# Kernel optimization log

Measured on AMD Instinct MI355X. Metric: run time of the kernel, lower is better.

## Reference

```python
import jax, jax.numpy as jnp
import numpy as np
from jax import lax

N, D_IN, D_H, D_A, N_CLS, K = 50000, 1024, 512, 256, 2, 8


def setup_inputs() -> dict:
    key = jax.random.key(0)
    ks = jax.random.split(key, 13)
    s = 0.02
    return {
        "h": jax.random.normal(ks[0], (1, N, D_IN), dtype=jnp.float32),
        "fc_W": jax.random.normal(ks[1], (D_H, D_IN), dtype=jnp.float32) * s,
        "fc_b": jnp.zeros((D_H,), jnp.float32),
        "att_a_W": jax.random.normal(ks[2], (D_A, D_H), dtype=jnp.float32) * s,
        "att_a_b": jnp.zeros((D_A,), jnp.float32),
        "att_b_W": jax.random.normal(ks[3], (D_A, D_H), dtype=jnp.float32) * s,
        "att_b_b": jnp.zeros((D_A,), jnp.float32),
        "att_c_W": jax.random.normal(ks[4], (1, D_A), dtype=jnp.float32) * s,
        "att_c_b": jnp.zeros((1,), jnp.float32),
        "cls_W": jax.random.normal(ks[5], (N_CLS, D_H), dtype=jnp.float32) * s,
        "cls_b": jnp.zeros((N_CLS,), jnp.float32),
        "inst_W": jax.random.normal(ks[6], (2, D_H), dtype=jnp.float32) * s,
        "inst_b": jnp.zeros((2,), jnp.float32),
        "label": 1,  # one_hot -> [0,1]: inst_eval runs only for classifier index 1
    }


def reference(h, fc_W, fc_b, att_a_W, att_a_b, att_b_W, att_b_b,
              att_c_W, att_c_b, cls_W, cls_b, inst_W, inst_b, label):
    x = jnp.squeeze(h, 0)                               # [N, 1024]
    hh = jax.nn.relu(x @ fc_W.T + fc_b)                 # [N, 512]
    # gated attention: tanh gate * sigmoid gate -> scalar score per instance
    a = jnp.tanh(hh @ att_a_W.T + att_a_b)              # [N, 256]
    b = jax.nn.sigmoid(hh @ att_b_W.T + att_b_b)        # [N, 256]
    A_raw = (a * b) @ att_c_W.T + att_c_b               # [N, 1]
    A = jax.nn.softmax(A_raw, axis=0)                   # softmax over instances

    # instance eval (label==1, subtyping=False -> only classifier index 1)
    scores = A_raw[:, 0]                                # [N]
    _, top_p_ids = lax.top_k(scores, K)
    _, top_n_ids = lax.top_k(-scores, K)
    ids = jnp.concatenate([top_p_ids, top_n_ids])       # [2K]
    inst = hh[ids]                                      # gather [2K, 512]
    logits = inst @ inst_W.T + inst_b                   # [2K, 2]
    targets = jnp.concatenate([jnp.ones((K,), jnp.int32),
                               jnp.zeros((K,), jnp.int32)])
    logp = jax.nn.log_softmax(logits, axis=-1)
    instance_loss = -jnp.mean(jnp.take_along_axis(logp, targets[:, None], axis=1))

    instance_scores = hh @ cls_W.T + cls_b              # [N, 2]
    preds = (instance_scores * A).sum(axis=0) / A.sum(axis=0)  # [2]
    preds = preds[None, :]                              # [1, 2]
    return preds, instance_scores, A_raw, instance_loss
```

## Files before the change

### kernel.cpp

```cpp
#include <hip/hip_runtime.h>
#include <hip/hip_bf16.h>
#include <math.h>

typedef __bf16 bf16_t;
typedef __bf16 bf16x4 __attribute__((ext_vector_type(4)));
typedef __bf16 bf16x8 __attribute__((ext_vector_type(8)));
typedef float  f32x4  __attribute__((ext_vector_type(4)));

#define NROWS 50000

typedef const __attribute__((address_space(1))) unsigned int* gp_t;
typedef __attribute__((address_space(3))) unsigned int* lp_t;
__device__ __forceinline__ void cp16(void* l, const void* g) {
    __builtin_amdgcn_global_load_lds((gp_t)g, (lp_t)l, 16, 0, 0);
}

__global__ void k_convert(const float* __restrict__ fcW,
                          const float* __restrict__ aW,
                          const float* __restrict__ bW,
                          bf16_t* __restrict__ permW1, bf16_t* __restrict__ permB2) {
    int t = blockIdx.x * 256 + threadIdx.x;
    if (t < 131072) {
        float4 v = *(const float4*)(fcW + (long)t * 4);
        int row = t >> 8;
        int k0 = (t & 255) * 4;
        int kt = k0 >> 5, q = (k0 >> 3) & 3, j = k0 & 7;
        bf16_t o[4] = {(bf16_t)v.x, (bf16_t)v.y, (bf16_t)v.z, (bf16_t)v.w};
        *(bf16x4*)(permW1 + kt * 16384 + q * 4096 + row * 8 + j) = *(bf16x4*)o;
    } else {
        int t2 = t - 131072;
        int isB = t2 >> 15;
        int f = t2 & 32767;
        float4 v = *(const float4*)(((isB ? bW : aW)) + (long)f * 4);
        int srow = f >> 7;
        int k0 = (f & 127) * 4;
        int kt = k0 >> 5, q = (k0 >> 3) & 3, j = k0 & 7;
        int r = ((srow >> 4) * 2 + isB) * 16 + (srow & 15);
        bf16_t o[4] = {(bf16_t)v.x, (bf16_t)v.y, (bf16_t)v.z, (bf16_t)v.w};
        *(bf16x4*)(permB2 + kt * 16384 + q * 4096 + r * 8 + j) = *(bf16x4*)o;
    }
}

__global__ __launch_bounds__(256, 4) void k_gemm1(
        const float* __restrict__ x, const bf16_t* __restrict__ permW1,
        const float* __restrict__ fcb, bf16_t* __restrict__ hh) {
    __shared__ __align__(16) char smem[32768];
    const int tid = threadIdx.x;
    const int w = tid >> 6, l = tid & 63, q = l >> 4, li = l & 15;
    const int wr = w >> 1, wc = w & 1;
    const int b = blockIdx.x;
    const int rtile = (b & 7) | ((b >> 5) << 3);
    const int ctile = (b >> 3) & 3;
    const long row0 = (long)rtile * 128;
    const int col0 = ctile * 128;

    f32x4 acc[4][4];
    #pragma unroll
    for (int a = 0; a < 4; a++)
        #pragma unroll
        for (int c = 0; c < 4; c++) acc[a][c] = (f32x4)0.0f;

    int arow[4], akx[4]; bool avalid[4];
    #pragma unroll
    for (int j = 0; j < 4; j++) {
        int s = j * 256 + tid;
        arow[j] = s >> 3; akx[j] = s & 7;
        avalid[j] = (row0 + arow[j]) < NROWS;
    }
    const float* xbase = x + row0 * 1024;

    float4 xv[4];
    #pragma unroll
    for (int j = 0; j < 4; j++)
        xv[j] = avalid[j] ? *(const float4*)(xbase + arow[j] * 1024 + akx[j] * 4)
                          : make_float4(0.f, 0.f, 0.f, 0.f);
    #pragma unroll
    for (int j = 0; j < 4; j++) {
        bf16_t o[4] = {(bf16_t)xv[j].x, (bf16_t)xv[j].y, (bf16_t)xv[j].z, (bf16_t)xv[j].w};
        *(bf16x4*)(smem + (akx[j] >> 1) * 2048 + arow[j] * 16 + (akx[j] & 1) * 8) = *(bf16x4*)o;
    }
    #pragma unroll
    for (int s2 = 0; s2 < 2; s2++) {
        int s = tid + s2 * 256;
        cp16(smem + 16384 + s * 16, permW1 + (s >> 7) * 4096 + (col0 + (s & 127)) * 8);
    }
    #pragma unroll
    for (int j = 0; j < 4; j++)
        xv[j] = avalid[j] ? *(const float4*)(xbase + arow[j] * 1024 + 32 + akx[j] * 4)
                          : make_float4(0.f, 0.f, 0.f, 0.f);
    __syncthreads();

    for (int kt = 0; kt < 32; kt++) {
        const int cur = kt & 1, nxt = cur ^ 1;
        if (kt < 31) {
            const bf16_t* gsrc = permW1 + (long)(kt + 1) * 16384;
            #pragma unroll
            for (int s2 = 0; s2 < 2; s2++) {
                int s = tid + s2 * 256;
                cp16(smem + 16384 + nxt * 8192 + s * 16, gsrc + (s >> 7) * 4096 + (col0 + (s & 127)) * 8);
            }
            #pragma unroll
            for (int j = 0; j < 4; j++) {
                bf16_t o[4] = {(bf16_t)xv[j].x, (bf16_t)xv[j].y, (bf16_t)xv[j].z, (bf16_t)xv[j].w};
                *(bf16x4*)(smem + nxt * 8192 + (akx[j] >> 1) * 2048 + arow[j] * 16 + (akx[j] & 1) * 8) = *(bf16x4*)o;
            }
            int kn = (kt < 30 ? kt + 2 : 31) * 32;
            #pragma unroll
            for (int j = 0; j < 4; j++)
                xv[j] = avalid[j] ? *(const float4*)(xbase + arow[j] * 1024 + kn + akx[j] * 4)
                                  : make_float4(0.f, 0.f, 0.f, 0.f);
        }
        const bf16_t* Ab = (const bf16_t*)(smem + cur * 8192);
        const bf16_t* Bb = (const bf16_t*)(smem + 16384 + cur * 8192);
        bf16x8 afr[4], bfr[4];
        #pragma unroll
        for (int tn = 0; tn < 4; tn++)
            bfr[tn] = *(const bf16x8*)(Bb + q * 1024 + (wc * 64 + tn * 16 + li) * 8);
        #pragma unroll
        for (int tm = 0; tm < 4; tm++)
            afr[tm] = *(const bf16x8*)(Ab + q * 1024 + (wr * 64 + tm * 16 + li) * 8);
        #pragma unroll
        for (int tm = 0; tm < 4; tm++)
            #pragma unroll
            for (int tn = 0; tn < 4; tn++)
                acc[tm][tn] = __builtin_amdgcn_mfma_f32_16x16x32_bf16(afr[tm], bfr[tn], acc[tm][tn], 0, 0, 0);
        __syncthreads();
    }

    bf16_t* t16 = (bf16_t*)smem;
    float bias[4];
    #pragma unroll
    for (int tn = 0; tn < 4; tn++) bias[tn] = fcb[col0 + wc * 64 + tn * 16 + li];
    const int rr = tid >> 3, cc = tid & 7;
    #pragma unroll
    for (int tm = 0; tm < 4; tm++) {
        #pragma unroll
        for (int tn = 0; tn < 4; tn++)
            #pragma unroll
            for (int r = 0; r < 4; r++) {
                float v = acc[tm][tn][r] + bias[tn];
                v = v > 0.f ? v : 0.f;
                t16[(wr * 16 + q * 4 + r) * 136 + wc * 64 + tn * 16 + li] = (bf16_t)v;
            }
        __syncthreads();
        long grow = row0 + ((rr >> 4) * 64) + tm * 16 + (rr & 15);
        if (grow < NROWS) {
            bf16x8 v0 = *(const bf16x8*)&t16[rr * 136 + cc * 16];
            bf16x8 v1 = *(const bf16x8*)&t16[rr * 136 + cc * 16 + 8];
            *(bf16x8*)&hh[grow * 512 + col0 + cc * 16] = v0;
            *(bf16x8*)&hh[grow * 512 + col0 + cc * 16 + 8] = v1;
        }
        __syncthreads();
    }
}

__global__ __launch_bounds__(512, 4) void k_gemm2(
        const bf16_t* __restrict__ hh, const bf16_t* __restrict__ permB2,
        const float* __restrict__ aab, const float* __restrict__ abb,
        const float* __restrict__ acW, const float* __restrict__ acb,
        const float* __restrict__ clsW, const float* __restrict__ clsb,
        float* __restrict__ Araw, float* __restrict__ inst) {
    __shared__ __align__(16) char smem[75776];
    bf16_t* cls_lds = (bf16_t*)(smem + 73728);

    const int tid = threadIdx.x;
    const int w = tid >> 6, l = tid & 63, q = l >> 4, li = l & 15;
    const long row0 = (long)blockIdx.x * 64;

    if (tid < 128) {
        int c = tid >> 6, k8 = (tid & 63) * 8;
        #pragma unroll
        for (int i = 0; i < 8; i++)
            cls_lds[c * 512 + k8 + i] = (bf16_t)clsW[c * 512 + k8 + i];
    }

    f32x4 acc[4][4];
    #pragma unroll
    for (int a = 0; a < 4; a++)
        #pragma unroll
        for (int c = 0; c < 4; c++) acc[a][c] = (f32x4)0.0f;
    float cls0[4] = {0.f,0.f,0.f,0.f}, cls1[4] = {0.f,0.f,0.f,0.f};

    {
        const bf16_t* gb = permB2 + (long)tid * 8;
        char* dst = smem + 8192 + tid * 16;
        #pragma unroll
        for (int j = 0; j < 4; j++) cp16(dst + j * 8192, gb + j * 4096);
        if (tid < 256) {
            const bf16_t* ga = hh + (row0 + (tid >> 2)) * 512 + (tid & 3) * 8;
            cp16(smem + tid * 16, ga);
        }
    }
    __syncthreads();

    for (int kt = 0; kt < 16; kt++) {
        const int cur = kt & 1, nxt = cur ^ 1;
        if (kt < 15) {
            const bf16_t* gb = permB2 + ((long)(kt + 1) * 2048 + tid) * 8;
            char* dst = smem + 8192 + nxt * 32768 + tid * 16;
            #pragma unroll
            for (int j = 0; j < 4; j++) cp16(dst + j * 8192, gb + j * 4096);
            if (tid < 256) {
                const bf16_t* ga = hh + (row0 + (tid >> 2)) * 512 + (kt + 1) * 32 + (tid & 3) * 8;
                cp16(smem + nxt * 4096 + tid * 16, ga);
            }
        }
        const bf16_t* asb = (const bf16_t*)(smem + cur * 4096);
        const bf16_t* bsb = (const bf16_t*)(smem + 8192 + cur * 32768);
        bf16x8 bfr[4];
        #pragma unroll
        for (int tn = 0; tn < 4; tn++)
            bfr[tn] = *(const bf16x8*)(bsb + q * 4096 + (w * 64 + tn * 16 + li) * 8);
        const bool mycls = ((kt >> 1) == w);
        bf16x8 w0, w1;
        if (mycls) {
            w0 = *(const bf16x8*)&cls_lds[kt * 32 + q * 8];
            w1 = *(const bf16x8*)&cls_lds[512 + kt * 32 + q * 8];
        }
        #pragma unroll
        for (int tm = 0; tm < 4; tm++) {
            bf16x8 af = *(const bf16x8*)(asb + (tm * 16 + li) * 32 + q * 8);
            #pragma unroll
            for (int tn = 0; tn < 4; tn++)
                acc[tm][tn] = __builtin_amdgcn_mfma_f32_16x16x32_bf16(af, bfr[tn], acc[tm][tn], 0, 0, 0);
            if (mycls) {
                float s0 = 0.f, s1 = 0.f;
                #pragma unroll
                for (int jj = 0; jj < 8; jj++) {
                    float a = (float)af[jj];
                    s0 += a * (float)w0[jj];
                    s1 += a * (float)w1[jj];
                }
                cls0[tm] += s0; cls1[tm] += s1;
            }
        }
        __syncthreads();
    }

    float (*apart)[9] = (float (*)[9])smem;
    float (*cls_part)[64][2] = (float (*)[64][2])(smem + 4096);

    float sum_mr[4][4];
    #pragma unroll
    for (int a = 0; a < 4; a++)
        #pragma unroll
        for (int c = 0; c < 4; c++) sum_mr[a][c] = 0.f;
    #pragma unroll
    for (int p = 0; p < 2; p++) {
        int j = (w * 2 + p) * 16 + li;
        float ab_ = aab[j], bb_ = abb[j], cw = acW[j];
        int tn_a = p * 2, tn_b = p * 2 + 1;
        #pragma unroll
        for (int tm = 0; tm < 4; tm++)
            #pragma unroll
            for (int r = 0; r < 4; r++) {
                float av = tanhf(acc[tm][tn_a][r] + ab_);
                float bv = acc[tm][tn_b][r] + bb_;
                bv = 1.f / (1.f + expf(-bv));
                sum_mr[tm][r] += av * bv * cw;
            }
    }
    #pragma unroll
    for (int tm = 0; tm < 4; tm++)
        #pragma unroll
        for (int r = 0; r < 4; r++) {
            float v = sum_mr[tm][r];
            v += __shfl_xor(v, 1); v += __shfl_xor(v, 2);
            v += __shfl_xor(v, 4); v += __shfl_xor(v, 8);
            if (li == 0) apart[tm * 16 + q * 4 + r][w] = v;
        }
    #pragma unroll
    for (int tm = 0; tm < 4; tm++) {
        cls0[tm] += __shfl_xor(cls0[tm], 16); cls0[tm] += __shfl_xor(cls0[tm], 32);
        cls1[tm] += __shfl_xor(cls1[tm], 16); cls1[tm] += __shfl_xor(cls1[tm], 32);
        if (q == 0) {
            cls_part[w][tm * 16 + li][0] = cls0[tm];
            cls_part[w][tm * 16 + li][1] = cls1[tm];
        }
    }
    __syncthreads();
    if (tid < 64) {
        float s = acb[0];
        #pragma unroll
        for (int ww = 0; ww < 8; ww++) s += apart[tid][ww];
        long row = row0 + tid;
        if (row < NROWS) Araw[row] = s;
    }
    if (tid < 128) {
        int rr = tid >> 1, c = tid & 1;
        float s = clsb[c];
        #pragma unroll
        for (int ww = 0; ww < 8; ww++) s += cls_part[ww][rr][c];
        long row = row0 + rr;
        if (row < NROWS) inst[row * 2 + c] = s;
    }
}

__global__ void k_topk_part(const float* __restrict__ scores,
                            float* __restrict__ candV, int* __restrict__ candI,
                            float* __restrict__ sums) {
    __shared__ float cv[4096];
    __shared__ int   ci[4096];
    __shared__ float bwv[8]; __shared__ int bwi[8]; __shared__ int bws[8];
    int tid = threadIdx.x;
    int p = blockIdx.x;
    if (p == 0 && tid == 0) { sums[0] = 0.f; sums[1] = 0.f; sums[2] = 0.f; }
    int lo = p * 6250, hi = lo + 6250;
    for (int pass = 0; pass < 2; pass++) {
        float sign = (pass == 0) ? 1.f : -1.f;
        float tv[8]; int ti[8];
        #pragma unroll
        for (int k = 0; k < 8; k++) { tv[k] = -1e30f; ti[k] = 0x7fffffff; }
        for (int i = lo + tid; i < hi; i += 512) {
            float v = sign * scores[i];
            if (v > tv[7] || (v == tv[7] && i < ti[7])) {
                int k = 7;
                while (k > 0 && (v > tv[k-1] || (v == tv[k-1] && i < ti[k-1]))) {
                    tv[k] = tv[k-1]; ti[k] = ti[k-1]; k--;
                }
                tv[k] = v; ti[k] = i;
            }
        }
        for (int k = 0; k < 8; k++) { cv[tid * 8 + k] = tv[k]; ci[tid * 8 + k] = ti[k]; }
        __syncthreads();
        for (int r = 0; r < 8; r++) {
            float bv = -1e30f; int bi = 0x7fffffff, bslot = 0;
            for (int j = 0; j < 8; j++) {
                int s = tid + 512 * j;
                float v = cv[s]; int idx = ci[s];
                if (v > bv || (v == bv && idx < bi)) { bv = v; bi = idx; bslot = s; }
            }
            for (int m = 1; m < 64; m <<= 1) {
                float ov = __shfl_xor(bv, m); int oi = __shfl_xor(bi, m); int os = __shfl_xor(bslot, m);
                if (ov > bv || (ov == bv && oi < bi)) { bv = ov; bi = oi; bslot = os; }
            }
            if ((tid & 63) == 0) { bwv[tid >> 6] = bv; bwi[tid >> 6] = bi; bws[tid >> 6] = bslot; }
            __syncthreads();
            if (tid == 0) {
                float BV = -1e30f; int BI = 0x7fffffff, BS = 0;
                for (int wv = 0; wv < 8; wv++) {
                    if (bwv[wv] > BV || (bwv[wv] == BV && bwi[wv] < BI)) { BV = bwv[wv]; BI = bwi[wv]; BS = bws[wv]; }
                }
                candV[pass * 64 + p * 8 + r] = BV;
                candI[pass * 64 + p * 8 + r] = BI;
                cv[BS] = -1e30f; ci[BS] = 0x7fffffff;
            }
            __syncthreads();
        }
        __syncthreads();
    }
}

__global__ void k_sum(const float* __restrict__ Araw, const float* __restrict__ inst,
                      const float* __restrict__ candV, float* sums) {
    __shared__ float r0[4], r1[4], r2[4];
    int tid = threadIdx.x;
    float mx = -1e30f;
    #pragma unroll
    for (int p = 0; p < 8; p++) mx = fmaxf(mx, candV[p * 8]);
    float se = 0.f, s0 = 0.f, s1 = 0.f;
    for (int i = blockIdx.x * 256 + tid; i < NROWS; i += 32768) {
        float e = expf(Araw[i] - mx);
        se += e; s0 += inst[2 * i] * e; s1 += inst[2 * i + 1] * e;
    }
    for (int s = 1; s < 64; s <<= 1) {
        se += __shfl_xor(se, s); s0 += __shfl_xor(s0, s); s1 += __shfl_xor(s1, s);
    }
    if ((tid & 63) == 0) { r0[tid >> 6] = se; r1[tid >> 6] = s0; r2[tid >> 6] = s1; }
    __syncthreads();
    if (tid == 0) {
        atomicAdd(&sums[0], r0[0] + r0[1] + r0[2] + r0[3]);
        atomicAdd(&sums[1], r1[0] + r1[1] + r1[2] + r1[3]);
        atomicAdd(&sums[2], r2[0] + r2[1] + r2[2] + r2[3]);
    }
}

__global__ void k_fin(const bf16_t* __restrict__ hh,
                      const float* __restrict__ candV, const int* __restrict__ candI,
                      const float* __restrict__ sums, const float* __restrict__ instW,
                      const float* __restrict__ instb, float* __restrict__ dout) {
    __shared__ int mid[16];
    __shared__ float lg[16][2];
    int tid = threadIdx.x;
    int wv = tid >> 6, l = tid & 63;
    if (wv < 2) {
        float v = candV[wv * 64 + l];
        int idx = candI[wv * 64 + l];
        for (int r = 0; r < 8; r++) {
            float bv = v; int bi = idx; int bs = l;
            for (int m = 1; m < 64; m <<= 1) {
                float ov = __shfl_xor(bv, m); int oi = __shfl_xor(bi, m); int os = __shfl_xor(bs, m);
                if (ov > bv || (ov == bv && oi < bi)) { bv = ov; bi = oi; bs = os; }
            }
            if (l == 0) mid[wv * 8 + r] = bi;
            if (l == bs) v = -1e30f;
        }
    }
    __syncthreads();
    int r = tid >> 4, li = tid & 15;
    int id = mid[r];
    const bf16_t* hp = hh + (long)id * 512;
    float p0 = 0.f, p1 = 0.f;
    for (int k = li * 32; k < li * 32 + 32; k++) {
        float h = (float)hp[k];
        p0 += h * instW[k]; p1 += h * instW[512 + k];
    }
    for (int m = 1; m < 16; m <<= 1) { p0 += __shfl_xor(p0, m); p1 += __shfl_xor(p1, m); }
    if (li == 0) { lg[r][0] = p0 + instb[0]; lg[r][1] = p1 + instb[1]; }
    __syncthreads();
    if (tid == 0) {
        float loss = 0.f;
        for (int r2 = 0; r2 < 16; r2++) {
            float l0 = lg[r2][0], l1 = lg[r2][1];
            float mx = fmaxf(l0, l1);
            float lse = mx + logf(expf(l0 - mx) + expf(l1 - mx));
            float lt = (r2 < 8) ? l1 : l0;
            loss += (lse - lt);
        }
        dout[150002] = loss / 16.f;
        float se = sums[0];
        dout[0] = sums[1] / se;
        dout[1] = sums[2] / se;
    }
}

extern "C" void kernel_launch(void* const* d_in, const int* in_sizes, int n_in,
                              void* d_out, int out_size, void* d_ws, size_t ws_size,
                              hipStream_t stream) {
    const float* h   = (const float*)d_in[0];
    const float* fcW = (const float*)d_in[1];
    const float* fcb = (const float*)d_in[2];
    const float* aaW = (const float*)d_in[3];
    const float* aab = (const float*)d_in[4];
    const float* abW = (const float*)d_in[5];
    const float* abb = (const float*)d_in[6];
    const float* acW = (const float*)d_in[7];
    const float* acb = (const float*)d_in[8];
    const float* clW = (const float*)d_in[9];
    const float* clb = (const float*)d_in[10];
    const float* inW = (const float*)d_in[11];
    const float* inb = (const float*)d_in[12];
    float* out = (float*)d_out;

    char* ws = (char*)d_ws;
    bf16_t* hh      = (bf16_t*)(ws);
    bf16_t* permW1  = (bf16_t*)(ws + 51200000);
    bf16_t* permB2  = (bf16_t*)(ws + 52248576);
    float*  candV   = (float*) (ws + 52772864);
    int*    candI   = (int*)   (ws + 52773888);
    float*  sums    = (float*) (ws + 52774912);

    float* inst = out + 2;
    float* Araw = out + 2 + 100000;

    k_convert<<<768, 256, 0, stream>>>(fcW, aaW, abW, permW1, permB2);
    k_gemm1<<<1568, 256, 0, stream>>>(h, permW1, fcb, hh);
    k_gemm2<<<782, 512, 0, stream>>>(hh, permB2, aab, abb, acW, acb, clW, clb, Araw, inst);
    k_topk_part<<<8, 512, 0, stream>>>(Araw, candV, candI, sums);
    k_sum<<<128, 256, 0, stream>>>(Araw, inst, candV, sums);
    k_fin<<<1, 256, 0, stream>>>(hh, candV, candI, sums, inW, inb, out);
}
```

Before: 488.1 us.

## Split attention GEMM across column halves with 128-row tiles and atomic score reduction

The attention GEMM now uses 256-thread blocks that each compute a 128-row tile over half of the 512 gate columns. The two halves combine the attention score with atomicAdd into a zeroed Araw buffer, and the classifier weights are pre-converted to bf16 once. Each block reuses every A-fragment across 8 B tiles and holds a smaller LDS footprint. In exchange it adds a memset, atomics, and reads hh twice. The top-k partial kernel now runs one pass per block over larger ranges and merges with a register-held sorted list instead of repeated block-wide syncs, so fewer candidates reach the final merge.

```diff
diff --git a/kernel.cpp b/kernel.cpp
--- a/kernel.cpp
+++ b/kernel.cpp
@@ -18,7 +18,9 @@
 __global__ void k_convert(const float* __restrict__ fcW,
                           const float* __restrict__ aW,
                           const float* __restrict__ bW,
-                          bf16_t* __restrict__ permW1, bf16_t* __restrict__ permB2) {
+                          const float* __restrict__ clsW,
+                          bf16_t* __restrict__ permW1, bf16_t* __restrict__ permB2,
+                          bf16_t* __restrict__ clsWb) {
     int t = blockIdx.x * 256 + threadIdx.x;
     if (t < 131072) {
         float4 v = *(const float4*)(fcW + (long)t * 4);
@@ -27,7 +29,7 @@
         int kt = k0 >> 5, q = (k0 >> 3) & 3, j = k0 & 7;
         bf16_t o[4] = {(bf16_t)v.x, (bf16_t)v.y, (bf16_t)v.z, (bf16_t)v.w};
         *(bf16x4*)(permW1 + kt * 16384 + q * 4096 + row * 8 + j) = *(bf16x4*)o;
-    } else {
+    } else if (t < 196608) {
         int t2 = t - 131072;
         int isB = t2 >> 15;
         int f = t2 & 32767;
@@ -38,6 +40,9 @@
         int r = ((srow >> 4) * 2 + isB) * 16 + (srow & 15);
         bf16_t o[4] = {(bf16_t)v.x, (bf16_t)v.y, (bf16_t)v.z, (bf16_t)v.w};
         *(bf16x4*)(permB2 + kt * 16384 + q * 4096 + r * 8 + j) = *(bf16x4*)o;
+    } else if (t < 197632) {
+        int i = t - 196608;
+        clsWb[i] = (bf16_t)clsW[i];
     }
 }
 
@@ -154,80 +159,82 @@
     }
 }
 
-__global__ __launch_bounds__(512, 4) void k_gemm2(
+__global__ __launch_bounds__(256, 2) void k_gemm2(
         const bf16_t* __restrict__ hh, const bf16_t* __restrict__ permB2,
+        const bf16_t* __restrict__ clsWb,
         const float* __restrict__ aab, const float* __restrict__ abb,
         const float* __restrict__ acW, const float* __restrict__ acb,
-        const float* __restrict__ clsW, const float* __restrict__ clsb,
+        const float* __restrict__ clsb,
         float* __restrict__ Araw, float* __restrict__ inst) {
-    __shared__ __align__(16) char smem[75776];
-    bf16_t* cls_lds = (bf16_t*)(smem + 73728);
+    __shared__ __align__(16) char smem[51200];
+    bf16_t* clsLds = (bf16_t*)(smem + 49152);
 
     const int tid = threadIdx.x;
     const int w = tid >> 6, l = tid & 63, q = l >> 4, li = l & 15;
-    const long row0 = (long)blockIdx.x * 64;
-
-    if (tid < 128) {
-        int c = tid >> 6, k8 = (tid & 63) * 8;
-        #pragma unroll
-        for (int i = 0; i < 8; i++)
-            cls_lds[c * 512 + k8 + i] = (bf16_t)clsW[c * 512 + k8 + i];
-    }
-
-    f32x4 acc[4][4];
+    const int wr = w >> 1, wc = w & 1;
+    const int b = blockIdx.x;
+    const int half = (b >= 391) ? 1 : 0;
+    const long row0 = (long)(half ? b - 391 : b) * 128;
+
+    f32x4 acc[4][8];
     #pragma unroll
     for (int a = 0; a < 4; a++)
         #pragma unroll
-        for (int c = 0; c < 4; c++) acc[a][c] = (f32x4)0.0f;
+        for (int c = 0; c < 8; c++) acc[a][c] = (f32x4)0.0f;
     float cls0[4] = {0.f,0.f,0.f,0.f}, cls1[4] = {0.f,0.f,0.f,0.f};
 
-    {
-        const bf16_t* gb = permB2 + (long)tid * 8;
-        char* dst = smem + 8192 + tid * 16;
-        #pragma unroll
-        for (int j = 0; j < 4; j++) cp16(dst + j * 8192, gb + j * 4096);
-        if (tid < 256) {
-            const bf16_t* ga = hh + (row0 + (tid >> 2)) * 512 + (tid & 3) * 8;
-            cp16(smem + tid * 16, ga);
-        }
+    if (tid < 128) cp16(smem + 49152 + tid * 16, clsWb + tid * 8);
+    #pragma unroll
+    for (int j = 0; j < 4; j++) {
+        int s = j * 256 + tid;
+        cp16(smem + 16384 + s * 16, permB2 + (s >> 8) * 4096 + (half * 256 + (s & 255)) * 8);
+    }
+    #pragma unroll
+    for (int j = 0; j < 2; j++) {
+        int s = j * 256 + tid;
+        cp16(smem + s * 16, hh + (row0 + (s >> 2)) * 512 + (s & 3) * 8);
     }
     __syncthreads();
 
     for (int kt = 0; kt < 16; kt++) {
         const int cur = kt & 1, nxt = cur ^ 1;
         if (kt < 15) {
-            const bf16_t* gb = permB2 + ((long)(kt + 1) * 2048 + tid) * 8;
-            char* dst = smem + 8192 + nxt * 32768 + tid * 16;
-            #pragma unroll
-            for (int j = 0; j < 4; j++) cp16(dst + j * 8192, gb + j * 4096);
-            if (tid < 256) {
-                const bf16_t* ga = hh + (row0 + (tid >> 2)) * 512 + (kt + 1) * 32 + (tid & 3) * 8;
-                cp16(smem + nxt * 4096 + tid * 16, ga);
-            }
-        }
-        const bf16_t* asb = (const bf16_t*)(smem + cur * 4096);
-        const bf16_t* bsb = (const bf16_t*)(smem + 8192 + cur * 32768);
-        bf16x8 bfr[4];
-        #pragma unroll
-        for (int tn = 0; tn < 4; tn++)
-            bfr[tn] = *(const bf16x8*)(bsb + q * 4096 + (w * 64 + tn * 16 + li) * 8);
-        const bool mycls = ((kt >> 1) == w);
-        bf16x8 w0, w1;
-        if (mycls) {
-            w0 = *(const bf16x8*)&cls_lds[kt * 32 + q * 8];
-            w1 = *(const bf16x8*)&cls_lds[512 + kt * 32 + q * 8];
-        }
-        #pragma unroll
-        for (int tm = 0; tm < 4; tm++) {
-            bf16x8 af = *(const bf16x8*)(asb + (tm * 16 + li) * 32 + q * 8);
-            #pragma unroll
-            for (int tn = 0; tn < 4; tn++)
-                acc[tm][tn] = __builtin_amdgcn_mfma_f32_16x16x32_bf16(af, bfr[tn], acc[tm][tn], 0, 0, 0);
-            if (mycls) {
+            const bf16_t* gb = permB2 + (long)(kt + 1) * 16384;
+            #pragma unroll
+            for (int j = 0; j < 4; j++) {
+                int s = j * 256 + tid;
+                cp16(smem + 16384 + nxt * 16384 + s * 16, gb + (s >> 8) * 4096 + (half * 256 + (s & 255)) * 8);
+            }
+            #pragma unroll
+            for (int j = 0; j < 2; j++) {
+                int s = j * 256 + tid;
+                cp16(smem + nxt * 8192 + s * 16, hh + (row0 + (s >> 2)) * 512 + (kt + 1) * 32 + (s & 3) * 8);
+            }
+        }
+        const bf16_t* Ab = (const bf16_t*)(smem + cur * 8192);
+        const bf16_t* Bb = (const bf16_t*)(smem + 16384 + cur * 16384);
+        bf16x8 bfr[8];
+        #pragma unroll
+        for (int tn = 0; tn < 8; tn++)
+            bfr[tn] = *(const bf16x8*)(Bb + q * 2048 + (wc * 128 + tn * 16 + li) * 8);
+        bf16x8 afr[4];
+        #pragma unroll
+        for (int tm = 0; tm < 4; tm++)
+            afr[tm] = *(const bf16x8*)(Ab + (wr * 64 + tm * 16 + li) * 32 + q * 8);
+        #pragma unroll
+        for (int tm = 0; tm < 4; tm++)
+            #pragma unroll
+            for (int tn = 0; tn < 8; tn++)
+                acc[tm][tn] = __builtin_amdgcn_mfma_f32_16x16x32_bf16(afr[tm], bfr[tn], acc[tm][tn], 0, 0, 0);
+        if (half == 0 && wc == (kt >> 3)) {
+            bf16x8 w0 = *(const bf16x8*)(clsLds + kt * 32 + q * 8);
+            bf16x8 w1 = *(const bf16x8*)(clsLds + 512 + kt * 32 + q * 8);
+            #pragma unroll
+            for (int tm = 0; tm < 4; tm++) {
                 float s0 = 0.f, s1 = 0.f;
                 #pragma unroll
                 for (int jj = 0; jj < 8; jj++) {
-                    float a = (float)af[jj];
+                    float a = (float)afr[tm][jj];
                     s0 += a * (float)w0[jj];
                     s1 += a * (float)w1[jj];
                 }
@@ -237,8 +244,8 @@
         __syncthreads();
     }
 
-    float (*apart)[9] = (float (*)[9])smem;
-    float (*cls_part)[64][2] = (float (*)[64][2])(smem + 4096);
+    float (*apart)[2]     = (float (*)[2])smem;
+    float (*cpart)[64][2] = (float (*)[64][2])(smem + 2048);
 
     float sum_mr[4][4];
     #pragma unroll
@@ -246,8 +253,8 @@
         #pragma unroll
         for (int c = 0; c < 4; c++) sum_mr[a][c] = 0.f;
     #pragma unroll
-    for (int p = 0; p < 2; p++) {
-        int j = (w * 2 + p) * 16 + li;
+    for (int p = 0; p < 4; p++) {
+        int j = (half * 8 + wc * 4 + p) * 16 + li;
         float ab_ = aab[j], bb_ = abb[j], cw = acW[j];
         int tn_a = p * 2, tn_b = p * 2 + 1;
         #pragma unroll
@@ -267,31 +274,30 @@
             float v = sum_mr[tm][r];
             v += __shfl_xor(v, 1); v += __shfl_xor(v, 2);
             v += __shfl_xor(v, 4); v += __shfl_xor(v, 8);
-            if (li == 0) apart[tm * 16 + q * 4 + r][w] = v;
-        }
-    #pragma unroll
-    for (int tm = 0; tm < 4; tm++) {
-        cls0[tm] += __shfl_xor(cls0[tm], 16); cls0[tm] += __shfl_xor(cls0[tm], 32);
-        cls1[tm] += __shfl_xor(cls1[tm], 16); cls1[tm] += __shfl_xor(cls1[tm], 32);
-        if (q == 0) {
-            cls_part[w][tm * 16 + li][0] = cls0[tm];
-            cls_part[w][tm * 16 + li][1] = cls1[tm];
-        }
-    }
-    __syncthreads();
-    if (tid < 64) {
-        float s = acb[0];
-        #pragma unroll
-        for (int ww = 0; ww < 8; ww++) s += apart[tid][ww];
+            if (li == 0) apart[wr * 64 + tm * 16 + q * 4 + r][wc] = v;
+        }
+    if (half == 0) {
+        #pragma unroll
+        for (int tm = 0; tm < 4; tm++) {
+            cls0[tm] += __shfl_xor(cls0[tm], 16); cls0[tm] += __shfl_xor(cls0[tm], 32);
+            cls1[tm] += __shfl_xor(cls1[tm], 16); cls1[tm] += __shfl_xor(cls1[tm], 32);
+            if (q == 0) {
+                cpart[w][tm * 16 + li][0] = cls0[tm];
+                cpart[w][tm * 16 + li][1] = cls1[tm];
+            }
+        }
+    }
+    __syncthreads();
+    if (tid < 128) {
+        float s = apart[tid][0] + apart[tid][1];
+        if (half == 0) s += acb[0];
         long row = row0 + tid;
-        if (row < NROWS) Araw[row] = s;
-    }
-    if (tid < 128) {
-        int rr = tid >> 1, c = tid & 1;
-        float s = clsb[c];
-        #pragma unroll
-        for (int ww = 0; ww < 8; ww++) s += cls_part[ww][rr][c];
-        long row = row0 + rr;
+        if (row < NROWS) atomicAdd(Araw + row, s);
+    }
+    if (half == 0) {
+        int r = tid >> 1, c = tid & 1;
+        float s = clsb[c] + cpart[2 * (r >> 6)][r & 63][c] + cpart[2 * (r >> 6) + 1][r & 63][c];
+        long row = row0 + r;
         if (row < NROWS) inst[row * 2 + c] = s;
     }
 }
@@ -301,53 +307,59 @@
                             float* __restrict__ sums) {
     __shared__ float cv[4096];
     __shared__ int   ci[4096];
-    __shared__ float bwv[8]; __shared__ int bwi[8]; __shared__ int bws[8];
     int tid = threadIdx.x;
     int p = blockIdx.x;
+    int pass = p & 1, rq = p >> 1;
     if (p == 0 && tid == 0) { sums[0] = 0.f; sums[1] = 0.f; sums[2] = 0.f; }
-    int lo = p * 6250, hi = lo + 6250;
-    for (int pass = 0; pass < 2; pass++) {
-        float sign = (pass == 0) ? 1.f : -1.f;
-        float tv[8]; int ti[8];
-        #pragma unroll
-        for (int k = 0; k < 8; k++) { tv[k] = -1e30f; ti[k] = 0x7fffffff; }
-        for (int i = lo + tid; i < hi; i += 512) {
-            float v = sign * scores[i];
-            if (v > tv[7] || (v == tv[7] && i < ti[7])) {
-                int k = 7;
-                while (k > 0 && (v > tv[k-1] || (v == tv[k-1] && i < ti[k-1]))) {
-                    tv[k] = tv[k-1]; ti[k] = ti[k-1]; k--;
-                }
-                tv[k] = v; ti[k] = i;
-            }
-        }
-        for (int k = 0; k < 8; k++) { cv[tid * 8 + k] = tv[k]; ci[tid * 8 + k] = ti[k]; }
-        __syncthreads();
+    float sign = pass ? -1.f : 1.f;
+    int lo = rq * 12500, hi = lo + 12500;
+    float tv[8]; int ti[8];
+    #pragma unroll
+    for (int k = 0; k < 8; k++) { tv[k] = -1e30f; ti[k] = 0x7fffffff; }
+    for (int i = lo + tid; i < hi; i += 512) {
+        float v = sign * scores[i];
+        if (v > tv[7] || (v == tv[7] && i < ti[7])) {
+            int k = 7;
+            while (k > 0 && (v > tv[k-1] || (v == tv[k-1] && i < ti[k-1]))) {
+                tv[k] = tv[k-1]; ti[k] = ti[k-1]; k--;
+            }
+            tv[k] = v; ti[k] = i;
+        }
+    }
+    #pragma unroll
+    for (int k = 0; k < 8; k++) { cv[tid * 8 + k] = tv[k]; ci[tid * 8 + k] = ti[k]; }
+    __syncthreads();
+    if (tid < 64) {
+        float mv[8]; int mi[8];
+        #pragma unroll
+        for (int k = 0; k < 8; k++) { mv[k] = -1e30f; mi[k] = 0x7fffffff; }
+        for (int i = 0; i < 64; i++) {
+            int slot = tid * 64 + ((i + tid) & 63);
+            float v = cv[slot]; int idx = ci[slot];
+            #pragma unroll
+            for (int k = 0; k < 8; k++) {
+                bool bt = (v > mv[k]) || (v == mv[k] && idx < mi[k]);
+                float nv = bt ? v : mv[k];  int ni = bt ? idx : mi[k];
+                float ov = bt ? mv[k] : v;  int oi = bt ? mi[k] : idx;
+                mv[k] = nv; mi[k] = ni; v = ov; idx = oi;
+            }
+        }
         for (int r = 0; r < 8; r++) {
-            float bv = -1e30f; int bi = 0x7fffffff, bslot = 0;
-            for (int j = 0; j < 8; j++) {
-                int s = tid + 512 * j;
-                float v = cv[s]; int idx = ci[s];
-                if (v > bv || (v == bv && idx < bi)) { bv = v; bi = idx; bslot = s; }
-            }
+            float bv = mv[0]; int bi = mi[0]; int bs = tid;
             for (int m = 1; m < 64; m <<= 1) {
-                float ov = __shfl_xor(bv, m); int oi = __shfl_xor(bi, m); int os = __shfl_xor(bslot, m);
-                if (ov > bv || (ov == bv && oi < bi)) { bv = ov; bi = oi; bslot = os; }
-            }
-            if ((tid & 63) == 0) { bwv[tid >> 6] = bv; bwi[tid >> 6] = bi; bws[tid >> 6] = bslot; }
-            __syncthreads();
+                float ov = __shfl_xor(bv, m); int oi = __shfl_xor(bi, m); int os = __shfl_xor(bs, m);
+                if (ov > bv || (ov == bv && oi < bi)) { bv = ov; bi = oi; bs = os; }
+            }
             if (tid == 0) {
-                float BV = -1e30f; int BI = 0x7fffffff, BS = 0;
-                for (int wv = 0; wv < 8; wv++) {
-                    if (bwv[wv] > BV || (bwv[wv] == BV && bwi[wv] < BI)) { BV = bwv[wv]; BI = bwi[wv]; BS = bws[wv]; }
-                }
-                candV[pass * 64 + p * 8 + r] = BV;
-                candI[pass * 64 + p * 8 + r] = BI;
-                cv[BS] = -1e30f; ci[BS] = 0x7fffffff;
-            }
-            __syncthreads();
-        }
-        __syncthreads();
+                candV[pass * 32 + rq * 8 + r] = bv;
+                candI[pass * 32 + rq * 8 + r] = bi;
+            }
+            if (tid == bs) {
+                #pragma unroll
+                for (int k = 0; k < 7; k++) { mv[k] = mv[k+1]; mi[k] = mi[k+1]; }
+                mv[7] = -1e30f; mi[7] = 0x7fffffff;
+            }
+        }
     }
 }
 
@@ -357,7 +369,7 @@
     int tid = threadIdx.x;
     float mx = -1e30f;
     #pragma unroll
-    for (int p = 0; p < 8; p++) mx = fmaxf(mx, candV[p * 8]);
+    for (int p = 0; p < 4; p++) mx = fmaxf(mx, candV[p * 8]);
     float se = 0.f, s0 = 0.f, s1 = 0.f;
     for (int i = blockIdx.x * 256 + tid; i < NROWS; i += 32768) {
         float e = expf(Araw[i] - mx);
@@ -384,8 +396,9 @@
     int tid = threadIdx.x;
     int wv = tid >> 6, l = tid & 63;
     if (wv < 2) {
-        float v = candV[wv * 64 + l];
-        int idx = candI[wv * 64 + l];
+        float v; int idx;
+        if (l < 32) { v = candV[wv * 32 + l]; idx = candI[wv * 32 + l]; }
+        else        { v = -1e30f; idx = 0x7fffffff; }
         for (int r = 0; r < 8; r++) {
             float bv = v; int bi = idx; int bs = l;
             for (int m = 1; m < 64; m <<= 1) {
@@ -393,7 +406,7 @@
                 if (ov > bv || (ov == bv && oi < bi)) { bv = ov; bi = oi; bs = os; }
             }
             if (l == 0) mid[wv * 8 + r] = bi;
-            if (l == bs) v = -1e30f;
+            if (l == bs) { v = -1e30f; idx = 0x7fffffff; }
         }
     }
     __syncthreads();
@@ -446,16 +459,18 @@
     bf16_t* hh      = (bf16_t*)(ws);
     bf16_t* permW1  = (bf16_t*)(ws + 51200000);
     bf16_t* permB2  = (bf16_t*)(ws + 52248576);
-    float*  candV   = (float*) (ws + 52772864);
-    int*    candI   = (int*)   (ws + 52773888);
-    float*  sums    = (float*) (ws + 52774912);
+    bf16_t* clsWb   = (bf16_t*)(ws + 52772864);
+    float*  candV   = (float*) (ws + 52774912);
+    int*    candI   = (int*)   (ws + 52775424);
+    float*  sums    = (float*) (ws + 52775936);
 
     float* inst = out + 2;
     float* Araw = out + 2 + 100000;
 
-    k_convert<<<768, 256, 0, stream>>>(fcW, aaW, abW, permW1, permB2);
+    k_convert<<<772, 256, 0, stream>>>(fcW, aaW, abW, clW, permW1, permB2, clsWb);
     k_gemm1<<<1568, 256, 0, stream>>>(h, permW1, fcb, hh);
-    k_gemm2<<<782, 512, 0, stream>>>(hh, permB2, aab, abb, acW, acb, clW, clb, Araw, inst);
+    hipMemsetAsync(Araw, 0, NROWS * sizeof(float), stream);
+    k_gemm2<<<782, 256, 0, stream>>>(hh, permB2, clsWb, aab, abb, acW, acb, clb, Araw, inst);
     k_topk_part<<<8, 512, 0, stream>>>(Araw, candV, candI, sums);
     k_sum<<<128, 256, 0, stream>>>(Araw, inst, candV, sums);
     k_fin<<<1, 256, 0, stream>>>(hh, candV, candI, sums, inW, inb, out);
```

Result: no change. 484.6 us (-0.7%).
